# Optimization experiments

Hardware: AMD Instinct MI355X
Metric: run time of the kernel (lower is better)

## Reference

```python
import jax, jax.numpy as jnp
import numpy as np

T, B, D, H, HH, OUT = 512, 128, 256, 1024, 256, 128
EPS = 1e-3

def _ln(x, gamma, beta):
    # layer_norm over feature dim, eps=0.001, matching torch reciprocal(sqrt(var+eps))
    m = jnp.mean(x, -1, keepdims=True)
    xs = x - m
    v = jnp.mean(xs * xs, -1, keepdims=True)
    return gamma * xs * jax.lax.rsqrt(v + EPS) + beta

def _ln_all(h, base, units, gamma, beta):
    # normalize each of `base` gate blocks independently over `units`
    b = h.shape[0]
    hr = h.reshape(b, base, units)
    m = jnp.mean(hr, -1, keepdims=True)
    xs = hr - m
    v = jnp.mean(xs * xs, -1, keepdims=True)
    hn = (xs * jax.lax.rsqrt(v + EPS)).reshape(b, base * units)
    return gamma * hn + beta

def setup_inputs() -> dict:
    key = jax.random.key(0)
    ks = jax.random.split(key, 12)
    return {
        "x": jax.random.normal(ks[0], (T, B, D), jnp.float32),
        "Wx": jax.random.normal(ks[1], (4 * H, D), jnp.float32) * (1.0 / np.sqrt(D)),
        "Wh": jax.random.normal(ks[2], (4 * H, H), jnp.float32) * (1.0 / np.sqrt(H)),
        "bias": jax.random.normal(ks[3], (4 * H,), jnp.float32) * 0.1,
        "lna_gamma": jnp.ones((4 * H,), jnp.float32),
        "lna_beta": jnp.zeros((4 * H,), jnp.float32),
        "ln_gamma": jnp.ones((H,), jnp.float32),
        "ln_beta": jnp.zeros((H,), jnp.float32),
        "zb": jax.random.normal(ks[4], (4, HH, HH), jnp.float32) * 0.01,   # ib/jb/fb/ob _zb
        "zbeta": jax.random.normal(ks[5], (4, HH, H), jnp.float32) * 0.01, # ib/jb/fb/ob _beta
        "zw_w": jax.random.normal(ks[6], (8, HH, HH), jnp.float32) * 0.01, # ix,jx,fx,ox,ih,jh,fh,oh _zw_w
        "zw_b": jnp.ones((8, HH), jnp.float32),
        "alpha": jnp.full((8, HH, H), 0.1 / HH, jnp.float32) + jax.random.normal(ks[7], (8, HH, H), jnp.float32) * 1e-4,
        "hyp_Wx": jax.random.normal(ks[8], (4 * HH, D + H), jnp.float32) * (1.0 / np.sqrt(D + H)),
        "hyp_bx": jnp.zeros((4 * HH,), jnp.float32),
        "hyp_Wh": jax.random.normal(ks[9], (4 * HH, HH), jnp.float32) * (1.0 / np.sqrt(HH)),
        "hyp_bh": jnp.zeros((4 * HH,), jnp.float32),
        "hyp_lna_gamma": jnp.ones((4 * HH,), jnp.float32),
        "hyp_lna_beta": jnp.zeros((4 * HH,), jnp.float32),
        "hyp_ln_gamma": jnp.ones((HH,), jnp.float32),
        "hyp_ln_beta": jnp.zeros((HH,), jnp.float32),
        "fc_W": jax.random.normal(ks[10], (OUT, H), jnp.float32) * (1.0 / np.sqrt(H)),
        "fc_b": jnp.zeros((OUT,), jnp.float32),
    }

def reference(x, Wx, Wh, bias, lna_gamma, lna_beta, ln_gamma, ln_beta, zb, zbeta,
              zw_w, zw_b, alpha, hyp_Wx, hyp_bx, hyp_Wh, hyp_bh,
              hyp_lna_gamma, hyp_lna_beta, hyp_ln_gamma, hyp_ln_beta, fc_W, fc_b):
    b4 = bias.reshape(4, H)

    def step(carry, xt):
        h, c, hh, ch = carry  # main (B,H), hyper (B,HH)
        # ---- hypernetwork LSTM cell (layer-norm LSTM) ----
        g = jnp.concatenate([xt, h], 1) @ hyp_Wx.T + hyp_bx + hh @ hyp_Wh.T + hyp_bh
        g = _ln_all(g, 4, HH, hyp_lna_gamma, hyp_lna_beta)
        hi, hf, hg, ho = jnp.split(g, 4, 1)  # ingate, forgetgate, cellgate, outgate
        ch_n = jax.nn.sigmoid(hf) * ch + jax.nn.sigmoid(hi) * jnp.tanh(hg)
        hyp = jax.nn.sigmoid(ho) * jnp.tanh(_ln(ch_n, hyp_ln_gamma, hyp_ln_beta))
        # ---- hyper-modulation: per-gate scale vectors and bias adjustments ----
        z = jnp.einsum('bq,kqp->kbp', hyp, zw_w) + zw_b[:, None, :]   # (8,B,HH)
        sc = jnp.einsum('kbp,kph->kbh', z, alpha)                     # (8,B,H)
        bz = jnp.einsum('bq,kqp->kbp', hyp, zb)                       # (4,B,HH)
        badj = jnp.einsum('kbp,kph->kbh', bz, zbeta)                  # (4,B,H)
        # ---- main LSTM gates (order i, j, f, o) ----
        xg = (xt @ Wx.T).reshape(B, 4, H).transpose(1, 0, 2)          # (4,B,H)
        hg2 = (h @ Wh.T).reshape(B, 4, H).transpose(1, 0, 2)          # (4,B,H)
        gates = sc[:4] * xg + sc[4:] * hg2 + b4[:, None, :] + badj    # (4,B,H)
        gates = _ln_all(gates.transpose(1, 0, 2).reshape(B, 4 * H), 4, H, lna_gamma, lna_beta)
        i, j, f, o = jnp.split(gates, 4, 1)
        c_n = jax.nn.sigmoid(f) * c + jax.nn.sigmoid(i) * jnp.tanh(j)
        h_n = jax.nn.sigmoid(o) * jnp.tanh(_ln(c_n, ln_gamma, ln_beta))
        return (h_n, c_n, hyp, ch_n), None

    init = (jnp.zeros((B, H), x.dtype), jnp.zeros((B, H), x.dtype),
            jnp.zeros((B, HH), x.dtype), jnp.zeros((B, HH), x.dtype))
    (h_f, _, _, _), _ = jax.lax.scan(step, init, x)
    return h_f @ fc_W.T + fc_b  # (B, OUT)
```

## Files before the change

### kernel.cpp

```cpp
#include <hip/hip_runtime.h>
#include <math.h>

#define T_STEPS 512
#define BATCH   128
#define DIN     256
#define HMAIN   1024
#define HHYP    256
#define OUTN    128
#define EPS     1e-3f

#define KSPLIT_NONE (1<<30)

typedef __attribute__((ext_vector_type(4))) float f32x4;
typedef __attribute__((ext_vector_type(8))) short s16x8;

__device__ __forceinline__ float sigm(float x){ return 1.f/(1.f + expf(-x)); }

__device__ __forceinline__ unsigned short f2bf(float f){
    union { float f; unsigned u; } x; x.f = f;
    unsigned r = x.u + 0x7FFFu + ((x.u >> 16) & 1u);
    return (unsigned short)(r >> 16);
}

#define BM 32
#define BN 64
#define KT 32
__device__ void gemm_dev(const float* __restrict__ A1, int lda1, int ksplit,
                         const float* __restrict__ A2, int lda2,
                         const float* __restrict__ Bp, int ldb, int b_nk,
                         const float* __restrict__ bias,
                         float* __restrict__ C, int ldc,
                         int K, int k0, int mtile, int ntile)
{
    __shared__ __align__(16) float As[KT][BM+4];
    __shared__ __align__(16) float Bs[KT][BN+4];
    const int tid = threadIdx.x;
    const int mt = tid >> 4, nt = tid & 15;
    const int m0g = mtile*BM, n0g = ntile*BN;
    float acc[4][4];
    #pragma unroll
    for (int i=0;i<4;++i) { acc[i][0]=0;acc[i][1]=0;acc[i][2]=0;acc[i][3]=0; }
    for (int kt = 0; kt < K; kt += KT) {
        __syncthreads();
        #pragma unroll
        for (int i=0;i<8;++i){
            int e = tid + i*128;
            int m = e >> 5, k = e & 31;
            int gk = k0 + kt + k, gm = m0g + m;
            float v = (gk < ksplit) ? A1[(size_t)gm*lda1 + gk]
                                    : A2[(size_t)gm*lda2 + (gk - ksplit)];
            As[k][m] = v;
        }
        if (b_nk) {
            #pragma unroll
            for (int i=0;i<16;++i){
                int e = tid + i*128;
                int n = e >> 5, k = e & 31;
                Bs[k][n] = Bp[(size_t)(n0g + n)*ldb + (k0 + kt + k)];
            }
        } else {
            #pragma unroll
            for (int i=0;i<16;++i){
                int e = tid + i*128;
                int k = e >> 6, n = e & 63;
                Bs[k][n] = Bp[(size_t)(k0 + kt + k)*ldb + (n0g + n)];
            }
        }
        __syncthreads();
        #pragma unroll
        for (int k=0;k<KT;++k){
            float4 av = *(const float4*)(&As[k][4*mt]);
            float4 bv = *(const float4*)(&Bs[k][4*nt]);
            acc[0][0]+=av.x*bv.x; acc[0][1]+=av.x*bv.y; acc[0][2]+=av.x*bv.z; acc[0][3]+=av.x*bv.w;
            acc[1][0]+=av.y*bv.x; acc[1][1]+=av.y*bv.y; acc[1][2]+=av.y*bv.z; acc[1][3]+=av.y*bv.w;
            acc[2][0]+=av.z*bv.x; acc[2][1]+=av.z*bv.y; acc[2][2]+=av.z*bv.z; acc[2][3]+=av.z*bv.w;
            acc[3][0]+=av.w*bv.x; acc[3][1]+=av.w*bv.y; acc[3][2]+=av.w*bv.z; acc[3][3]+=av.w*bv.w;
        }
    }
    #pragma unroll
    for (int i=0;i<4;++i){
        int gm = m0g + 4*mt + i;
        #pragma unroll
        for (int j=0;j<4;++j){
            int gn = n0g + 4*nt + j;
            float v = acc[i][j];
            if (bias) v += bias[gn];
            C[(size_t)gm*ldc + gn] = v;
        }
    }
}

#define ASTR 40
__device__ void gemm_mfma(const float* __restrict__ A1, int lda1, int ksplit,
                          const float* __restrict__ A2, int lda2,
                          const unsigned short* __restrict__ B, int ldb,
                          const float* __restrict__ bias,
                          float* __restrict__ C, int ldc,
                          int K, int k0, int mtile, int ntile)
{
    __shared__ __align__(16) unsigned short As[32*ASTR];
    __shared__ __align__(16) unsigned short Bs[128*ASTR];
    const int tid = threadIdx.x;
    const int lane = tid & 63, w = tid >> 6;
    const int wm = (w >> 1) * 16, wn = (w & 1) * 64;
    const int fr = lane & 15, koff = (lane >> 4) * 8;
    const int m0g = mtile*32, n0g = ntile*128;

    f32x4 acc[4];
    #pragma unroll
    for (int j=0;j<4;++j) acc[j] = (f32x4){0.f,0.f,0.f,0.f};

    const int arow = tid >> 3, akc = (tid & 7) * 4;
    for (int kt = 0; kt < K; kt += 32) {
        __syncthreads();
        {
            int gk = k0 + kt + akc;
            int gm = m0g + arow;
            const float* src = (gk < ksplit) ? (A1 + (size_t)gm*lda1 + gk)
                                             : (A2 + (size_t)gm*lda2 + (gk - ksplit));
            float4 v = *(const float4*)src;
            unsigned short* d = &As[arow*ASTR + akc];
            d[0] = f2bf(v.x); d[1] = f2bf(v.y); d[2] = f2bf(v.z); d[3] = f2bf(v.w);
        }
        #pragma unroll
        for (int i=0;i<4;++i){
            int e = tid + i*256;
            int n = e >> 3, kc = (e & 7) * 4;
            ushort4 bv = *(const ushort4*)(B + (size_t)(n0g + n)*ldb + (k0 + kt + kc));
            unsigned short* d = &Bs[n*ASTR + kc];
            d[0] = bv.x; d[1] = bv.y; d[2] = bv.z; d[3] = bv.w;
        }
        __syncthreads();
        s16x8 af = *(const s16x8*)&As[(wm + fr)*ASTR + koff];
        #pragma unroll
        for (int j=0;j<4;++j){
            s16x8 bf = *(const s16x8*)&Bs[(wn + j*16 + fr)*ASTR + koff];
            acc[j] = __builtin_amdgcn_mfma_f32_16x16x32_bf16(af, bf, acc[j], 0, 0, 0);
        }
    }
    #pragma unroll
    for (int j=0;j<4;++j){
        int gn = n0g + wn + j*16 + fr;
        float bb = bias ? bias[gn] : 0.f;
        #pragma unroll
        for (int r=0;r<4;++r){
            int gm = m0g + wm + (lane >> 4)*4 + r;
            C[(size_t)gm*ldc + gn] = acc[j][r] + bb;
        }
    }
}

__global__ __launch_bounds__(256) void k_prep_convert(
    const float* __restrict__ hyp_Wx, const float* __restrict__ hyp_Wh,
    const float* __restrict__ hyp_bx, const float* __restrict__ hyp_bh,
    const float* __restrict__ Wx, const float* __restrict__ Wh,
    unsigned short* __restrict__ wcat1bf, unsigned short* __restrict__ wxbf,
    unsigned short* __restrict__ whbf, float* __restrict__ bias1,
    float* __restrict__ act1, float* __restrict__ c, float* __restrict__ ch)
{
    size_t i = (size_t)blockIdx.x*256 + threadIdx.x;
    if (i < 1572864u) {
        int n = (int)(i / 1536), k = (int)(i % 1536);
        float v = (k < 1280) ? hyp_Wx[(size_t)n*1280 + k] : hyp_Wh[(size_t)n*256 + (k-1280)];
        wcat1bf[i] = f2bf(v); return;
    }
    i -= 1572864u;
    if (i < 1048576u) { wxbf[i] = f2bf(Wx[i]); return; }
    i -= 1048576u;
    if (i < 4194304u) { whbf[i] = f2bf(Wh[i]); return; }
    i -= 4194304u;
    if (i < 1024u) { bias1[i] = hyp_bx[i] + hyp_bh[i]; return; }
    i -= 1024u;
    if (i < 163840u) { act1[i] = 0.f; return; }
    i -= 163840u;
    if (i < 131072u) { c[i] = 0.f; return; }
    i -= 131072u;
    if (i < 32768u) { ch[i] = 0.f; return; }
}

__global__ __launch_bounds__(128) void k_prep_wcomb(
    const float* __restrict__ zw_w, const float* __restrict__ zb,
    const float* __restrict__ alpha, const float* __restrict__ zbeta,
    float* __restrict__ wcombf32)
{
    int kk = blockIdx.z;
    const float* A = (kk < 8) ? (zw_w + (size_t)kk*65536) : (zb + (size_t)(kk-8)*65536);
    const float* Bm = (kk < 8) ? (alpha + (size_t)kk*262144) : (zbeta + (size_t)(kk-8)*262144);
    gemm_dev(A, 256, KSPLIT_NONE, A, 256, Bm, 1024, 0, nullptr,
             wcombf32 + (size_t)kk*262144, 1024, 256, 0, blockIdx.x, blockIdx.y);
}

__global__ __launch_bounds__(256) void k_prep_cvtcomb(
    const float* __restrict__ wcombf32, unsigned short* __restrict__ wcombbf)
{
    size_t i = (size_t)blockIdx.x*256 + threadIdx.x;
    if (i >= 3145728u) return;
    int kk = (int)(i / 262144u);
    int r  = (int)(i % 262144u);
    int n = r / 256, k = r % 256;
    wcombbf[i] = f2bf(wcombf32[(size_t)kk*262144 + (size_t)k*1024 + n]);
}

__global__ __launch_bounds__(256) void k_prep_bcomb(
    const float* __restrict__ zw_b, const float* __restrict__ alpha,
    float* __restrict__ bcomb)
{
    int k = blockIdx.x;
    int n = blockIdx.y*256 + threadIdx.x;
    float s = 0.f;
    for (int p=0;p<256;++p)
        s += zw_b[k*256+p] * alpha[(size_t)k*262144 + (size_t)p*1024 + n];
    bcomb[(size_t)k*1024 + n] = s;
}

__global__ __launch_bounds__(256) void k_step1(
    const float* __restrict__ xt, const float* __restrict__ act1,
    const unsigned short* __restrict__ wcat1bf,
    const unsigned short* __restrict__ wxbf, const unsigned short* __restrict__ whbf,
    float* __restrict__ gpart, float* __restrict__ xghg)
{
    int bid = blockIdx.x;
    if (bid < 128) {
        int sp = bid >> 5, r = bid & 31;
        gemm_mfma(xt, 256, 256, act1, 1280, wcat1bf, 1536, nullptr,
                  gpart + (size_t)sp*131072, 1024, 384, sp*384, r >> 3, r & 7);
    } else if (bid < 256) {
        int r = bid - 128;
        gemm_mfma(xt, 256, KSPLIT_NONE, xt, 256, wxbf, 256, nullptr,
                  xghg, 4096, 256, 0, r >> 5, r & 31);
    } else {
        int r = bid - 256;
        gemm_mfma(act1, 1280, KSPLIT_NONE, act1, 1280, whbf, 1024, nullptr,
                  xghg + 524288, 4096, 1024, 0, r >> 5, r & 31);
    }
}

__global__ __launch_bounds__(256) void k_step2(
    const float* __restrict__ act1, const unsigned short* __restrict__ wcombbf,
    const float* __restrict__ bcomb, float* __restrict__ scb)
{
    int bid = blockIdx.x;
    int kk = bid >> 5, r = bid & 31;
    const float* bias = (kk < 8) ? (bcomb + (size_t)kk*1024) : nullptr;
    gemm_mfma(act1 + 1024, 1280, KSPLIT_NONE, act1 + 1024, 1280,
              wcombbf + (size_t)kk*262144, 256, bias,
              scb + (size_t)kk*131072, 1024, 256, 0, r >> 3, r & 7);
}

__device__ __forceinline__ void breduce2(float& a, float& b, volatile float* buf, int tid){
    #pragma unroll
    for (int off = 32; off > 0; off >>= 1) { a += __shfl_xor(a, off); b += __shfl_xor(b, off); }
    __syncthreads();
    if ((tid & 63) == 0) { buf[(tid>>6)*2] = a; buf[(tid>>6)*2+1] = b; }
    __syncthreads();
    a = buf[0] + buf[2] + buf[4] + buf[6];
    b = buf[1] + buf[3] + buf[5] + buf[7];
}

__global__ __launch_bounds__(256) void k_hyper_cell(
    const float* __restrict__ lna_g, const float* __restrict__ lna_b,
    const float* __restrict__ ln_g, const float* __restrict__ ln_b,
    const float* __restrict__ gpart, const float* __restrict__ bias1,
    float* __restrict__ ch, float* __restrict__ act1)
{
    __shared__ float buf[8];
    int b = blockIdx.x, tid = threadIdx.x;
    float v[4];
    #pragma unroll
    for (int g=0; g<4; ++g){
        int idx = b*1024 + g*256 + tid;
        v[g] = gpart[idx] + gpart[131072 + idx] + gpart[262144 + idx] + gpart[393216 + idx]
             + bias1[g*256 + tid];
    }
    #pragma unroll
    for (int g=0; g<4; ++g){
        float s = v[g], ss = v[g]*v[g];
        breduce2(s, ss, buf, tid);
        float m = s * (1.f/256.f);
        float var = ss * (1.f/256.f) - m*m;
        v[g] = (v[g]-m)*rsqrtf(var + EPS)*lna_g[g*256+tid] + lna_b[g*256+tid];
    }
    float chp = ch[b*256 + tid];
    float cn = sigm(v[1])*chp + sigm(v[0])*tanhf(v[2]);
    float s = cn, ss = cn*cn;
    breduce2(s, ss, buf, tid);
    float m = s*(1.f/256.f);
    float var = ss*(1.f/256.f) - m*m;
    float hn = sigm(v[3]) * tanhf((cn-m)*rsqrtf(var + EPS)*ln_g[tid] + ln_b[tid]);
    ch[b*256 + tid] = cn;
    act1[b*1280 + 1024 + tid] = hn;
}

__global__ __launch_bounds__(256) void k_main_cell(
    const float* __restrict__ bias4,
    const float* __restrict__ lna_g, const float* __restrict__ lna_b,
    const float* __restrict__ ln_g, const float* __restrict__ ln_b,
    const float* __restrict__ xghg, const float* __restrict__ scb,
    float* __restrict__ c, float* __restrict__ act1)
{
    __shared__ float buf[8];
    int b = blockIdx.x, tid = threadIdx.x;
    float gn[4][4];
    #pragma unroll
    for (int k=0;k<4;++k){
        float pre[4]; float s=0.f, ss=0.f;
        #pragma unroll
        for (int j=0;j<4;++j){
            int h = j*256 + tid;
            int n = k*1024 + h;
            int bh = b*1024 + h;
            float xgv = xghg[b*4096 + n];
            float hgv = xghg[524288 + b*4096 + n];
            float p = scb[k*131072 + bh]*xgv + scb[(4+k)*131072 + bh]*hgv
                    + bias4[n] + scb[(8+k)*131072 + bh];
            pre[j] = p; s += p; ss += p*p;
        }
        breduce2(s, ss, buf, tid);
        float m = s*(1.f/1024.f);
        float var = ss*(1.f/1024.f) - m*m;
        float rs = rsqrtf(var + EPS);
        #pragma unroll
        for (int j=0;j<4;++j){
            int h=j*256+tid, n=k*1024+h;
            gn[k][j] = (pre[j]-m)*rs*lna_g[n] + lna_b[n];
        }
    }
    float cnv[4]; float s=0.f, ss=0.f;
    #pragma unroll
    for (int j=0;j<4;++j){
        int h=j*256+tid;
        float cv = c[b*1024+h];
        float x = sigm(gn[2][j])*cv + sigm(gn[0][j])*tanhf(gn[1][j]);
        cnv[j]=x; s+=x; ss+=x*x;
    }
    breduce2(s, ss, buf, tid);
    float m=s*(1.f/1024.f);
    float var=ss*(1.f/1024.f)-m*m;
    float rs=rsqrtf(var + EPS);
    #pragma unroll
    for (int j=0;j<4;++j){
        int h=j*256+tid;
        float hv = sigm(gn[3][j])*tanhf((cnv[j]-m)*rs*ln_g[h] + ln_b[h]);
        c[b*1024+h] = cnv[j];
        act1[b*1280 + h] = hv;
    }
}

__global__ __launch_bounds__(128) void k_fc(
    const float* __restrict__ fcW, const float* __restrict__ fcb,
    const float* __restrict__ act1, float* __restrict__ out)
{
    int b = blockIdx.x, o = threadIdx.x;
    const float* h = act1 + (size_t)b*1280;
    float s = fcb[o];
    for (int k=0;k<1024;++k) s += h[k]*fcW[(size_t)o*1024 + k];
    out[b*OUTN + o] = s;
}

extern "C" void kernel_launch(void* const* d_in, const int* in_sizes, int n_in,
                              void* d_out, int out_size, void* d_ws, size_t ws_size,
                              hipStream_t stream)
{
    const float* x        = (const float*)d_in[0];
    const float* Wx       = (const float*)d_in[1];
    const float* Wh       = (const float*)d_in[2];
    const float* bias     = (const float*)d_in[3];
    const float* lna_g    = (const float*)d_in[4];
    const float* lna_b    = (const float*)d_in[5];
    const float* ln_g     = (const float*)d_in[6];
    const float* ln_b     = (const float*)d_in[7];
    const float* zb       = (const float*)d_in[8];
    const float* zbeta    = (const float*)d_in[9];
    const float* zw_w     = (const float*)d_in[10];
    const float* zw_b     = (const float*)d_in[11];
    const float* alpha    = (const float*)d_in[12];
    const float* hyp_Wx   = (const float*)d_in[13];
    const float* hyp_bx   = (const float*)d_in[14];
    const float* hyp_Wh   = (const float*)d_in[15];
    const float* hyp_bh   = (const float*)d_in[16];
    const float* hlna_g   = (const float*)d_in[17];
    const float* hlna_b   = (const float*)d_in[18];
    const float* hln_g    = (const float*)d_in[19];
    const float* hln_b    = (const float*)d_in[20];
    const float* fcW      = (const float*)d_in[21];
    const float* fcb      = (const float*)d_in[22];
    float* out = (float*)d_out;

    unsigned short* wcat1bf = (unsigned short*)d_ws;
    unsigned short* wxbf    = wcat1bf + 1572864;
    unsigned short* whbf    = wxbf + 1048576;
    unsigned short* wcombbf = whbf + 4194304;
    float* bcomb = (float*)(wcombbf + 3145728);
    float* bias1 = bcomb + 8192;
    float* act1  = bias1 + 1024;
    float* c     = act1 + 163840;
    float* ch    = c + 131072;
    float* stepbuf = ch + 32768;
    float* gpart = stepbuf;
    float* scb   = gpart + 524288;
    float* xghg  = scb + 1572864;
    float* wcombf32 = stepbuf;

    k_prep_convert<<<(7144448 + 255)/256, 256, 0, stream>>>(
        hyp_Wx, hyp_Wh, hyp_bx, hyp_bh, Wx, Wh,
        wcat1bf, wxbf, whbf, bias1, act1, c, ch);
    k_prep_wcomb<<<dim3(8,16,12), 128, 0, stream>>>(zw_w, zb, alpha, zbeta, wcombf32);
    k_prep_bcomb<<<dim3(8,4), 256, 0, stream>>>(zw_b, alpha, bcomb);
    k_prep_cvtcomb<<<(3145728 + 255)/256, 256, 0, stream>>>(wcombf32, wcombbf);

    for (int t = 0; t < T_STEPS; ++t) {
        const float* xt = x + (size_t)t*BATCH*DIN;
        k_step1<<<384, 256, 0, stream>>>(xt, act1, wcat1bf, wxbf, whbf, gpart, xghg);
        k_hyper_cell<<<BATCH, 256, 0, stream>>>(hlna_g, hlna_b, hln_g, hln_b,
                                                gpart, bias1, ch, act1);
        k_step2<<<384, 256, 0, stream>>>(act1, wcombbf, bcomb, scb);
        k_main_cell<<<BATCH, 256, 0, stream>>>(bias, lna_g, lna_b, ln_g, ln_b,
                                               xghg, scb, c, act1);
    }

    k_fc<<<BATCH, 128, 0, stream>>>(fcW, fcb, act1, out);
}
```

Before: 34.17 ms.

## Fuse per-timestep kernel launches into a persistent cooperative kernel with grid syncs

Replaces the four kernel launches per timestep (2048 launches in total) with a single cooperative persistent kernel of 384 blocks. The kernel loops over timesteps and separates the GEMM and cell phases with grid-wide barriers. The cell bodies are moved into shared device functions, and the old multi-launch path is kept as a fallback when cooperative launch or occupancy is insufficient. This is meant to remove per-launch overhead and the gaps between dependent kernels, at the cost of grid.sync latency and an occupancy cap of 2 blocks per CU.

```diff
diff --git a/kernel.cpp b/kernel.cpp
--- a/kernel.cpp
+++ b/kernel.cpp
@@ -1,5 +1,8 @@
 #include <hip/hip_runtime.h>
+#include <hip/hip_cooperative_groups.h>
 #include <math.h>
+
+namespace cg = cooperative_groups;
 
 #define T_STEPS 512
 #define BATCH   128
@@ -213,6 +216,103 @@
     bcomb[(size_t)k*1024 + n] = s;
 }
 
+__device__ __forceinline__ void breduce2(float& a, float& b, volatile float* buf, int tid){
+    #pragma unroll
+    for (int off = 32; off > 0; off >>= 1) { a += __shfl_xor(a, off); b += __shfl_xor(b, off); }
+    __syncthreads();
+    if ((tid & 63) == 0) { buf[(tid>>6)*2] = a; buf[(tid>>6)*2+1] = b; }
+    __syncthreads();
+    a = buf[0] + buf[2] + buf[4] + buf[6];
+    b = buf[1] + buf[3] + buf[5] + buf[7];
+}
+
+__device__ __forceinline__ void hyper_cell_body(
+    const float* __restrict__ lna_g, const float* __restrict__ lna_b,
+    const float* __restrict__ ln_g, const float* __restrict__ ln_b,
+    const float* __restrict__ gpart, const float* __restrict__ bias1,
+    float* __restrict__ ch, float* __restrict__ act1, int b, int tid)
+{
+    __shared__ float buf[8];
+    float v[4];
+    #pragma unroll
+    for (int g=0; g<4; ++g){
+        int idx = b*1024 + g*256 + tid;
+        v[g] = gpart[idx] + gpart[131072 + idx] + gpart[262144 + idx] + gpart[393216 + idx]
+             + bias1[g*256 + tid];
+    }
+    #pragma unroll
+    for (int g=0; g<4; ++g){
+        float s = v[g], ss = v[g]*v[g];
+        breduce2(s, ss, buf, tid);
+        float m = s * (1.f/256.f);
+        float var = ss * (1.f/256.f) - m*m;
+        v[g] = (v[g]-m)*rsqrtf(var + EPS)*lna_g[g*256+tid] + lna_b[g*256+tid];
+    }
+    float chp = ch[b*256 + tid];
+    float cn = sigm(v[1])*chp + sigm(v[0])*tanhf(v[2]);
+    float s = cn, ss = cn*cn;
+    breduce2(s, ss, buf, tid);
+    float m = s*(1.f/256.f);
+    float var = ss*(1.f/256.f) - m*m;
+    float hn = sigm(v[3]) * tanhf((cn-m)*rsqrtf(var + EPS)*ln_g[tid] + ln_b[tid]);
+    ch[b*256 + tid] = cn;
+    act1[b*1280 + 1024 + tid] = hn;
+}
+
+__device__ __forceinline__ void main_cell_body(
+    const float* __restrict__ bias4,
+    const float* __restrict__ lna_g, const float* __restrict__ lna_b,
+    const float* __restrict__ ln_g, const float* __restrict__ ln_b,
+    const float* __restrict__ xghg, const float* __restrict__ scb,
+    float* __restrict__ c, float* __restrict__ act1, int b, int tid)
+{
+    __shared__ float buf[8];
+    float gn[4][4];
+    #pragma unroll
+    for (int k=0;k<4;++k){
+        float pre[4]; float s=0.f, ss=0.f;
+        #pragma unroll
+        for (int j=0;j<4;++j){
+            int h = j*256 + tid;
+            int n = k*1024 + h;
+            int bh = b*1024 + h;
+            float xgv = xghg[b*4096 + n];
+            float hgv = xghg[524288 + b*4096 + n];
+            float p = scb[k*131072 + bh]*xgv + scb[(4+k)*131072 + bh]*hgv
+                    + bias4[n] + scb[(8+k)*131072 + bh];
+            pre[j] = p; s += p; ss += p*p;
+        }
+        breduce2(s, ss, buf, tid);
+        float m = s*(1.f/1024.f);
+        float var = ss*(1.f/1024.f) - m*m;
+        float rs = rsqrtf(var + EPS);
+        #pragma unroll
+        for (int j=0;j<4;++j){
+            int h=j*256+tid, n=k*1024+h;
+            gn[k][j] = (pre[j]-m)*rs*lna_g[n] + lna_b[n];
+        }
+    }
+    float cnv[4]; float s=0.f, ss=0.f;
+    #pragma unroll
+    for (int j=0;j<4;++j){
+        int h=j*256+tid;
+        float cv = c[b*1024+h];
+        float x = sigm(gn[2][j])*cv + sigm(gn[0][j])*tanhf(gn[1][j]);
+        cnv[j]=x; s+=x; ss+=x*x;
+    }
+    breduce2(s, ss, buf, tid);
+    float m=s*(1.f/1024.f);
+    float var=ss*(1.f/1024.f)-m*m;
+    float rs=rsqrtf(var + EPS);
+    #pragma unroll
+    for (int j=0;j<4;++j){
+        int h=j*256+tid;
+        float hv = sigm(gn[3][j])*tanhf((cnv[j]-m)*rs*ln_g[h] + ln_b[h]);
+        c[b*1024+h] = cnv[j];
+        act1[b*1280 + h] = hv;
+    }
+}
+
 __global__ __launch_bounds__(256) void k_step1(
     const float* __restrict__ xt, const float* __restrict__ act1,
     const unsigned short* __restrict__ wcat1bf,
@@ -247,48 +347,14 @@
               scb + (size_t)kk*131072, 1024, 256, 0, r >> 3, r & 7);
 }
 
-__device__ __forceinline__ void breduce2(float& a, float& b, volatile float* buf, int tid){
-    #pragma unroll
-    for (int off = 32; off > 0; off >>= 1) { a += __shfl_xor(a, off); b += __shfl_xor(b, off); }
-    __syncthreads();
-    if ((tid & 63) == 0) { buf[(tid>>6)*2] = a; buf[(tid>>6)*2+1] = b; }
-    __syncthreads();
-    a = buf[0] + buf[2] + buf[4] + buf[6];
-    b = buf[1] + buf[3] + buf[5] + buf[7];
-}
-
 __global__ __launch_bounds__(256) void k_hyper_cell(
     const float* __restrict__ lna_g, const float* __restrict__ lna_b,
     const float* __restrict__ ln_g, const float* __restrict__ ln_b,
     const float* __restrict__ gpart, const float* __restrict__ bias1,
     float* __restrict__ ch, float* __restrict__ act1)
 {
-    __shared__ float buf[8];
-    int b = blockIdx.x, tid = threadIdx.x;
-    float v[4];
-    #pragma unroll
-    for (int g=0; g<4; ++g){
-        int idx = b*1024 + g*256 + tid;
-        v[g] = gpart[idx] + gpart[131072 + idx] + gpart[262144 + idx] + gpart[393216 + idx]
-             + bias1[g*256 + tid];
-    }
-    #pragma unroll
-    for (int g=0; g<4; ++g){
-        float s = v[g], ss = v[g]*v[g];
-        breduce2(s, ss, buf, tid);
-        float m = s * (1.f/256.f);
-        float var = ss * (1.f/256.f) - m*m;
-        v[g] = (v[g]-m)*rsqrtf(var + EPS)*lna_g[g*256+tid] + lna_b[g*256+tid];
-    }
-    float chp = ch[b*256 + tid];
-    float cn = sigm(v[1])*chp + sigm(v[0])*tanhf(v[2]);
-    float s = cn, ss = cn*cn;
-    breduce2(s, ss, buf, tid);
-    float m = s*(1.f/256.f);
-    float var = ss*(1.f/256.f) - m*m;
-    float hn = sigm(v[3]) * tanhf((cn-m)*rsqrtf(var + EPS)*ln_g[tid] + ln_b[tid]);
-    ch[b*256 + tid] = cn;
-    act1[b*1280 + 1024 + tid] = hn;
+    hyper_cell_body(lna_g, lna_b, ln_g, ln_b, gpart, bias1, ch, act1,
+                    blockIdx.x, threadIdx.x);
 }
 
 __global__ __launch_bounds__(256) void k_main_cell(
@@ -298,51 +364,65 @@
     const float* __restrict__ xghg, const float* __restrict__ scb,
     float* __restrict__ c, float* __restrict__ act1)
 {
-    __shared__ float buf[8];
-    int b = blockIdx.x, tid = threadIdx.x;
-    float gn[4][4];
-    #pragma unroll
-    for (int k=0;k<4;++k){
-        float pre[4]; float s=0.f, ss=0.f;
-        #pragma unroll
-        for (int j=0;j<4;++j){
-            int h = j*256 + tid;
-            int n = k*1024 + h;
-            int bh = b*1024 + h;
-            float xgv = xghg[b*4096 + n];
-            float hgv = xghg[524288 + b*4096 + n];
-            float p = scb[k*131072 + bh]*xgv + scb[(4+k)*131072 + bh]*hgv
-                    + bias4[n] + scb[(8+k)*131072 + bh];
-            pre[j] = p; s += p; ss += p*p;
-        }
-        breduce2(s, ss, buf, tid);
-        float m = s*(1.f/1024.f);
-        float var = ss*(1.f/1024.f) - m*m;
-        float rs = rsqrtf(var + EPS);
-        #pragma unroll
-        for (int j=0;j<4;++j){
-            int h=j*256+tid, n=k*1024+h;
-            gn[k][j] = (pre[j]-m)*rs*lna_g[n] + lna_b[n];
-        }
-    }
-    float cnv[4]; float s=0.f, ss=0.f;
-    #pragma unroll
-    for (int j=0;j<4;++j){
-        int h=j*256+tid;
-        float cv = c[b*1024+h];
-        float x = sigm(gn[2][j])*cv + sigm(gn[0][j])*tanhf(gn[1][j]);
-        cnv[j]=x; s+=x; ss+=x*x;
-    }
-    breduce2(s, ss, buf, tid);
-    float m=s*(1.f/1024.f);
-    float var=ss*(1.f/1024.f)-m*m;
-    float rs=rsqrtf(var + EPS);
-    #pragma unroll
-    for (int j=0;j<4;++j){
-        int h=j*256+tid;
-        float hv = sigm(gn[3][j])*tanhf((cnv[j]-m)*rs*ln_g[h] + ln_b[h]);
-        c[b*1024+h] = cnv[j];
-        act1[b*1280 + h] = hv;
+    main_cell_body(bias4, lna_g, lna_b, ln_g, ln_b, xghg, scb, c, act1,
+                   blockIdx.x, threadIdx.x);
+}
+
+__global__ __launch_bounds__(256, 2) void k_persistent(
+    const float* __restrict__ x,
+    const unsigned short* __restrict__ wcat1bf,
+    const unsigned short* __restrict__ wxbf,
+    const unsigned short* __restrict__ whbf,
+    const unsigned short* __restrict__ wcombbf,
+    const float* __restrict__ bcomb,
+    const float* __restrict__ bias1,
+    const float* __restrict__ bias4,
+    const float* __restrict__ lna_g, const float* __restrict__ lna_b,
+    const float* __restrict__ ln_g, const float* __restrict__ ln_b,
+    const float* __restrict__ hlna_g, const float* __restrict__ hlna_b,
+    const float* __restrict__ hln_g, const float* __restrict__ hln_b,
+    float* __restrict__ gpart, float* __restrict__ scb,
+    float* __restrict__ xghg, float* __restrict__ act1,
+    float* __restrict__ c, float* __restrict__ ch)
+{
+    cg::grid_group grid = cg::this_grid();
+    const int bid = blockIdx.x;
+    const int tid = threadIdx.x;
+
+    for (int t = 0; t < T_STEPS; ++t) {
+        const float* xt = x + (size_t)t*BATCH*DIN;
+
+        if (bid < 128) {
+            int sp = bid >> 5, r = bid & 31;
+            gemm_mfma(xt, 256, 256, act1, 1280, wcat1bf, 1536, nullptr,
+                      gpart + (size_t)sp*131072, 1024, 384, sp*384, r >> 3, r & 7);
+        } else if (bid < 256) {
+            int r = bid - 128;
+            gemm_mfma(xt, 256, KSPLIT_NONE, xt, 256, wxbf, 256, nullptr,
+                      xghg, 4096, 256, 0, r >> 5, r & 31);
+        } else {
+            int r = bid - 256;
+            gemm_mfma(act1, 1280, KSPLIT_NONE, act1, 1280, whbf, 1024, nullptr,
+                      xghg + 524288, 4096, 1024, 0, r >> 5, r & 31);
+        }
+        grid.sync();
+
+        if (bid < 128)
+            hyper_cell_body(hlna_g, hlna_b, hln_g, hln_b, gpart, bias1, ch, act1, bid, tid);
+        grid.sync();
+
+        {
+            int kk = bid >> 5, r = bid & 31;
+            const float* bias = (kk < 8) ? (bcomb + (size_t)kk*1024) : nullptr;
+            gemm_mfma(act1 + 1024, 1280, KSPLIT_NONE, act1 + 1024, 1280,
+                      wcombbf + (size_t)kk*262144, 256, bias,
+                      scb + (size_t)kk*131072, 1024, 256, 0, r >> 3, r & 7);
+        }
+        grid.sync();
+
+        if (bid < 128)
+            main_cell_body(bias4, lna_g, lna_b, ln_g, ln_b, xghg, scb, c, act1, bid, tid);
+        grid.sync();
     }
 }
 
@@ -408,14 +488,55 @@
     k_prep_bcomb<<<dim3(8,4), 256, 0, stream>>>(zw_b, alpha, bcomb);
     k_prep_cvtcomb<<<(3145728 + 255)/256, 256, 0, stream>>>(wcombf32, wcombbf);
 
-    for (int t = 0; t < T_STEPS; ++t) {
-        const float* xt = x + (size_t)t*BATCH*DIN;
-        k_step1<<<384, 256, 0, stream>>>(xt, act1, wcat1bf, wxbf, whbf, gpart, xghg);
-        k_hyper_cell<<<BATCH, 256, 0, stream>>>(hlna_g, hlna_b, hln_g, hln_b,
-                                                gpart, bias1, ch, act1);
-        k_step2<<<384, 256, 0, stream>>>(act1, wcombbf, bcomb, scb);
-        k_main_cell<<<BATCH, 256, 0, stream>>>(bias, lna_g, lna_b, ln_g, ln_b,
-                                               xghg, scb, c, act1);
+    static int use_coop = -1;
+    if (use_coop < 0) {
+        use_coop = 0;
+        int dev = 0;
+        if (hipGetDevice(&dev) == hipSuccess) {
+            hipDeviceProp_t prop;
+            if (hipGetDeviceProperties(&prop, dev) == hipSuccess &&
+                prop.cooperativeLaunch) {
+                int occ = 0;
+                if (hipOccupancyMaxActiveBlocksPerMultiprocessor(
+                        &occ, (const void*)k_persistent, 256, 0) == hipSuccess &&
+                    occ * prop.multiProcessorCount >= 384) {
+                    use_coop = 1;
+                }
+            }
+        }
+    }
+
+    int coop_launched = 0;
+    if (use_coop) {
+        void* cargs[] = {
+            (void*)&x, (void*)&wcat1bf, (void*)&wxbf, (void*)&whbf, (void*)&wcombbf,
+            (void*)&bcomb, (void*)&bias1, (void*)&bias,
+            (void*)&lna_g, (void*)&lna_b, (void*)&ln_g, (void*)&ln_b,
+            (void*)&hlna_g, (void*)&hlna_b, (void*)&hln_g, (void*)&hln_b,
+            (void*)&gpart, (void*)&scb, (void*)&xghg, (void*)&act1,
+            (void*)&c, (void*)&ch
+        };
+        hipError_t e = hipLaunchCooperativeKernel((const void*)k_persistent,
+                                                  dim3(384), dim3(256),
+                                                  cargs, 0u, stream);
+        if (e == hipSuccess) {
+            coop_launched = 1;
+        } else {
+            (void)hipGetLastError();
+            use_coop = 0;
+        }
+    }
+
+    if (!coop_launched) {
+        for (int t = 0; t < T_STEPS; ++t) {
+            const float* xt = x + (size_t)t*BATCH*DIN;
+            k_step1<<<384, 256, 0, stream>>>(xt, act1, wcat1bf, wxbf, whbf, gpart, xghg);
+            k_hyper_cell<<<BATCH, 256, 0, stream>>>(hlna_g, hlna_b, hln_g, hln_b,
+                                                    gpart, bias1, ch, act1);
+            k_step2<<<384, 256, 0, stream>>>(act1, wcombbf, bcomb, scb);
+            k_main_cell<<<BATCH, 256, 0, stream>>>(bias, lna_g, lna_b, ln_g, ln_b,
+                                                   xghg, scb, c, act1);
+        }
     }
 
     k_fc<<<BATCH, 128, 0, stream>>>(fcW, fcb, act1, out);
```

Measured after the change: 34.28 ms. About the same (+0.3%).
